# Optimization experiments

Measured on AMD Instinct MI355X. Metric: run time of the kernel, lower is better.

## Reference

```python
import jax, jax.numpy as jnp
import numpy as np

EMB_DIM = 1024
HEAD = 16
HEAD_DIM = EMB_DIM // HEAD


def setup_inputs() -> dict:
    key = jax.random.key(0)
    ks = jax.random.split(key, 6)
    s = 1.0 / np.sqrt(EMB_DIM)
    return {
        "z": jax.random.normal(ks[0], (4, 2048, EMB_DIM), dtype=jnp.float32),
        "w_q": jax.random.normal(ks[1], (EMB_DIM, EMB_DIM), dtype=jnp.float32) * s,
        "w_k": jax.random.normal(ks[2], (EMB_DIM, EMB_DIM), dtype=jnp.float32) * s,
        "w_v": jax.random.normal(ks[3], (EMB_DIM, EMB_DIM), dtype=jnp.float32) * s,
        "w_o": jax.random.normal(ks[4], (EMB_DIM, EMB_DIM), dtype=jnp.float32) * s,
        "b_o": jax.random.normal(ks[5], (EMB_DIM,), dtype=jnp.float32) * 0.01,
    }


def reference(z, w_q, w_k, w_v, w_o, b_o):
    B, N, D = z.shape
    # QKV projections (nn.Linear: x @ W.T; here weights stored as (D_in, D_out))
    q = (z @ w_q).reshape(B, N, HEAD, HEAD_DIM).transpose(0, 2, 1, 3)  # bhnd
    k = (z @ w_k).reshape(B, N, HEAD, HEAD_DIM).transpose(0, 2, 1, 3)
    v = (z @ w_v).reshape(B, N, HEAD, HEAD_DIM).transpose(0, 2, 1, 3)
    scale = 1.0 / np.sqrt(HEAD_DIM).astype(np.float32)
    dots = jnp.einsum("bhnd,bhmd->bhnm", q, k) * scale
    attn = jax.nn.softmax(dots, axis=-1)
    out = jnp.einsum("bhnm,bhmd->bhnd", attn, v)
    out = out.transpose(0, 2, 1, 3).reshape(B, N, D)
    return out @ w_o + b_o
```

## Files before the change

### kernel.cpp

```cpp
#include <hip/hip_runtime.h>
#include <hip/hip_bf16.h>
#include <stdint.h>

typedef unsigned short u16;
typedef __attribute__((ext_vector_type(8))) short bf16x8;
typedef __attribute__((ext_vector_type(4))) float f32x4;
typedef __attribute__((ext_vector_type(16))) float f32x16;

static __device__ inline u16 f2bf(float f) {
  union { float f; uint32_t u; } v; v.f = f;
  uint32_t u = v.u;
  u += 0x7fffu + ((u >> 16) & 1);
  return (u16)(u >> 16);
}

static __device__ inline float fast_exp2(float x) {
#if __has_builtin(__builtin_amdgcn_exp2f)
  return __builtin_amdgcn_exp2f(x);
#else
  return __expf(x * 0.6931471805599453f);
#endif
}

static __device__ inline uint32_t pack_bf16(float lo, float hi) {
#if __has_builtin(__builtin_amdgcn_cvt_pk_bf16_f32)
  typedef __attribute__((ext_vector_type(2))) __bf16 bf16x2_t;
  bf16x2_t r = __builtin_amdgcn_cvt_pk_bf16_f32(lo, hi);
  union { bf16x2_t v; uint32_t u; } c; c.v = r;
  return c.u;
#else
  union { float f; uint32_t u; } a, b;
  a.f = lo; b.f = hi;
  uint32_t ua = a.u + 0x8000u;
  uint32_t ub = b.u + 0x8000u;
  return __builtin_amdgcn_perm(ub, ua, 0x07060302u);
#endif
}

static __device__ __forceinline__ void plswap(uint32_t a, uint32_t b,
                                              uint32_t& x, uint32_t& y) {
#if __has_builtin(__builtin_amdgcn_permlane32_swap)
  auto r = __builtin_amdgcn_permlane32_swap(a, b, false, false);
  x = (uint32_t)r[0]; y = (uint32_t)r[1];
#else
  int h = (threadIdx.x & 63) >> 5;
  uint32_t pa = (uint32_t)__shfl_xor((int)a, 32, 64);
  uint32_t pb = (uint32_t)__shfl_xor((int)b, 32, 64);
  x = h ? pb : a;
  y = h ? b : pa;
#endif
}

static __device__ __forceinline__ void load_lds_128(const u16* g, u16* l) {
  __builtin_amdgcn_global_load_lds((const __attribute__((address_space(1))) void*)g,
                                   (__attribute__((address_space(3))) void*)l,
                                   16, 0, 0);
}

__global__ __launch_bounds__(256) void prep_kernel(const float* __restrict__ zsrc,
                                                   u16* __restrict__ zdst,
                                                   const float* __restrict__ wq,
                                                   const float* __restrict__ wk,
                                                   const float* __restrict__ wv,
                                                   const float* __restrict__ wo,
                                                   u16* __restrict__ bqkv,
                                                   u16* __restrict__ wot) {
  const int bid = blockIdx.x;
  const int tid = threadIdx.x;
  if (bid < 8192) {
    int i = bid * 256 + tid;
    float4 v = reinterpret_cast<const float4*>(zsrc)[i];
    uint2 o;
    o.x = pack_bf16(v.x, v.y);
    o.y = pack_bf16(v.z, v.w);
    reinterpret_cast<uint2*>(zdst)[i] = o;
    return;
  }
  const int w = bid - 8192;
  const int z = w >> 10;
  const int rem = w & 1023;
  const float* src = (z == 0) ? wq : (z == 1) ? wk : (z == 2) ? wv : wo;
  u16* dst = (z < 3) ? (bqkv + (size_t)z * 1024 * 1024) : wot;
  __shared__ float tile[32][33];
  const int c0 = (rem & 31) * 32, r0 = (rem >> 5) * 32;
  const int tx = tid & 31, ty = tid >> 5;
#pragma unroll
  for (int i = 0; i < 32; i += 8)
    tile[ty + i][tx] = src[(size_t)(r0 + ty + i) * 1024 + c0 + tx];
  __syncthreads();
#pragma unroll
  for (int i = 0; i < 32; i += 8)
    dst[(size_t)(c0 + ty + i) * 1024 + r0 + tx] = f2bf(tile[tx][ty + i]);
}

__global__ __launch_bounds__(256) void gemm_bt64_kernel(
    const u16* __restrict__ A, const u16* __restrict__ Bt,
    float* __restrict__ outC, const float* __restrict__ bias) {
  const int Kd = 1024;
  const int n0 = blockIdx.x * 64;
  const int m0 = blockIdx.y * 128;
  __shared__ __align__(16) u16 Asm[128 * 32];
  __shared__ __align__(16) u16 Bsm[64 * 32];
  const int tid = threadIdx.x;
  const int wave = tid >> 6, lane = tid & 63;
  const int quad = lane >> 4, l15 = lane & 15;
  const int wm = (wave >> 1) * 64, wn = (wave & 1) * 32;

  const int c0 = wave * 128 + lane;
  const int c1 = c0 + 64;
  const int r0 = c0 >> 2, p0 = (c0 & 3) * 8;
  const int r1 = c1 >> 2, p1 = (c1 & 3) * 8;
  const int cB = tid;
  const int rB = cB >> 2, pB = (cB & 3) * 8;

  const u16* Ab = A + (size_t)m0 * Kd;
  const u16* Bb = Bt + (size_t)n0 * Kd;

  f32x4 acc[4][2] = {};

  for (int k0 = 0; k0 < Kd; k0 += 32) {
    __syncthreads();
    load_lds_128(Ab + (size_t)r0 * Kd + k0 + p0, Asm + c0 * 8);
    load_lds_128(Ab + (size_t)r1 * Kd + k0 + p1, Asm + c1 * 8);
    load_lds_128(Bb + (size_t)rB * Kd + k0 + pB, Bsm + cB * 8);
    __syncthreads();
    bf16x8 af[4], bf[2];
#pragma unroll
    for (int i = 0; i < 4; i++)
      af[i] = *reinterpret_cast<const bf16x8*>(Asm + (wm + i * 16 + l15) * 32 + quad * 8);
#pragma unroll
    for (int i = 0; i < 2; i++)
      bf[i] = *reinterpret_cast<const bf16x8*>(Bsm + (wn + i * 16 + l15) * 32 + quad * 8);
#pragma unroll
    for (int mi = 0; mi < 4; mi++)
#pragma unroll
      for (int ni = 0; ni < 2; ni++)
        acc[mi][ni] = __builtin_amdgcn_mfma_f32_16x16x32_bf16(af[mi], bf[ni], acc[mi][ni], 0, 0, 0);
  }

#pragma unroll
  for (int mi = 0; mi < 4; mi++)
#pragma unroll
    for (int ni = 0; ni < 2; ni++) {
      int n = n0 + wn + ni * 16 + l15;
      float bv = bias[n];
#pragma unroll
      for (int r = 0; r < 4; r++) {
        int m = m0 + wm + mi * 16 + quad * 4 + r;
        outC[(size_t)m * 1024 + n] = acc[mi][ni][r] + bv;
      }
    }
}

__global__ __launch_bounds__(512, 2) void gemm256_kernel(
    const u16* __restrict__ A, const u16* __restrict__ Bt,
    u16* __restrict__ outQ, u16* __restrict__ outK, u16* __restrict__ outVt) {
  const int tid = threadIdx.x;
  const int lane = tid & 63;
  const int wave = tid >> 6;
  const int quad = lane >> 4, l15 = lane & 15;
  const int e15 = l15 & 7;
  const int wm = wave >> 2;
  const int wn = wave & 3;

  unsigned lin = blockIdx.y * gridDim.x + blockIdx.x;
  unsigned nwg = gridDim.x * gridDim.y;
  lin = (lin & 7u) * (nwg >> 3) + (lin >> 3);
  const int bx = lin % gridDim.x, by = lin / gridDim.x;
  const int n0 = bx * 256, m0 = by * 256;

  __shared__ __align__(16) u16 AsmL[2][16384];
  __shared__ __align__(16) u16 BsmL[2][16384];
  u16* const As_[2] = {&AsmL[0][0], &AsmL[1][0]};
  u16* const Bs_[2] = {&BsmL[0][0], &BsmL[1][0]};

  const u16* Abase = A + (size_t)m0 * 1024;
  const u16* Bbase = Bt + (size_t)n0 * 1024;

  const int awoff = wm * 8192;
  const int bwoff = (wn >> 1) * 8192 + (wn & 1) * 4096;

  f32x4 acc[8][4] = {};
  bf16x8 af[4][2], bfr[4][2];

#define STG_HALF(ldsp, gp)                                                      \
  {                                                                             \
    const int cs0 = tid, cs1 = tid + 512;                                       \
    const int r0_ = cs0 >> 3, g0_ = (((cs0 & 7) ^ (r0_ & 7)) << 3);             \
    const int r1_ = cs1 >> 3, g1_ = (((cs1 & 7) ^ (r1_ & 7)) << 3);             \
    load_lds_128((gp) + (size_t)r0_ * 1024 + g0_, (ldsp) + cs0 * 8);            \
    load_lds_128((gp) + (size_t)r1_ * 1024 + g1_, (ldsp) + cs1 * 8);            \
  }

#define PHB() do { asm volatile("" ::: "memory"); __builtin_amdgcn_s_barrier(); \
                   asm volatile("" ::: "memory"); } while (0)
#define LGKM0() do { asm volatile("s_waitcnt lgkmcnt(0)" ::: "memory");         \
                     __builtin_amdgcn_sched_barrier(0); } while (0)
#define VMC8()  asm volatile("s_waitcnt vmcnt(8)" ::: "memory")

#define RD_A(mb, B)                                                             \
  _Pragma("unroll") for (int x = 0; x < 4; x++)                                 \
  _Pragma("unroll") for (int kk = 0; kk < 2; kk++)                              \
    af[x][kk] = *reinterpret_cast<const bf16x8*>(                               \
        As_[B] + awoff + (((mb) + x) * 16 + l15) * 64 + (((quad + kk * 4) ^ e15) << 3));

#define RD_B(nb, B)                                                             \
  _Pragma("unroll") for (int x = 0; x < 2; x++)                                 \
  _Pragma("unroll") for (int kk = 0; kk < 2; kk++)                              \
    bfr[(nb) + x][kk] = *reinterpret_cast<const bf16x8*>(                       \
        Bs_[B] + bwoff + (((nb) + x) * 16 + l15) * 64 + (((quad + kk * 4) ^ e15) << 3));

#define MM(mb, nb)                                                              \
  _Pragma("unroll") for (int kk = 0; kk < 2; kk++)                              \
  _Pragma("unroll") for (int x = 0; x < 4; x++)                                 \
  _Pragma("unroll") for (int y = 0; y < 2; y++)                                 \
    acc[(mb) + x][(nb) + y] = __builtin_amdgcn_mfma_f32_16x16x32_bf16(          \
        af[x][kk], bfr[(nb) + y][kk], acc[(mb) + x][(nb) + y], 0, 0, 0);

#define TILE4(B, KS)                                                            \
  RD_A(0, B); RD_B(0, B);                                                       \
  PHB(); LGKM0(); __builtin_amdgcn_s_setprio(1); MM(0, 0);                      \
  __builtin_amdgcn_s_setprio(0); PHB();                                         \
  RD_B(2, B);                                                                   \
  PHB(); LGKM0(); __builtin_amdgcn_s_setprio(1); MM(0, 2);                      \
  __builtin_amdgcn_s_setprio(0); PHB();                                         \
  RD_A(4, B);                                                                   \
  STG_HALF(Bs_[B], Bbase + (KS)); STG_HALF(Bs_[B] + 8192, Bbase + 128 * 1024 + (KS)); \
  PHB(); LGKM0(); __builtin_amdgcn_s_setprio(1); MM(4, 0);                      \
  __builtin_amdgcn_s_setprio(0); PHB();                                         \
  STG_HALF(As_[B], Abase + (KS)); STG_HALF(As_[B] + 8192, Abase + 128 * 1024 + (KS)); \
  PHB(); __builtin_amdgcn_s_setprio(1); MM(4, 2);                               \
  __builtin_amdgcn_s_setprio(0); VMC8(); PHB();

  STG_HALF(As_[0], Abase);      STG_HALF(As_[0] + 8192, Abase + 128 * 1024);
  STG_HALF(Bs_[0], Bbase);      STG_HALF(Bs_[0] + 8192, Bbase + 128 * 1024);
  STG_HALF(As_[1], Abase + 64); STG_HALF(As_[1] + 8192, Abase + 128 * 1024 + 64);
  STG_HALF(Bs_[1], Bbase + 64); STG_HALF(Bs_[1] + 8192, Bbase + 128 * 1024 + 64);
  VMC8(); PHB();

#pragma unroll 1
  for (int it = 0; it < 8; ++it) {
    int t2 = it * 2 + 2; if (t2 > 15) t2 = 15;
    int t3 = it * 2 + 3; if (t3 > 15) t3 = 15;
    const int k2 = t2 * 64, k3 = t3 * 64;
    TILE4(0, k2);
    TILE4(1, k3);
  }

  const int which = (n0 + wn * 64) >> 10;
#pragma unroll
  for (int mi = 0; mi < 8; mi++)
#pragma unroll
    for (int ni = 0; ni < 4; ni++) {
      int n = n0 + wn * 64 + ni * 16 + l15;
      int hn = n & 1023;
      int hh = hn >> 6, dim = hn & 63;
      if (which == 2) {
        int m = m0 + wm * 128 + mi * 16 + quad * 4;
        int b = m >> 11, tok = m & 2047;
        uint2 pk;
        pk.x = pack_bf16(acc[mi][ni][0], acc[mi][ni][1]);
        pk.y = pack_bf16(acc[mi][ni][2], acc[mi][ni][3]);
        *reinterpret_cast<uint2*>(outVt + ((size_t)(b * 16 + hh) * 64 + dim) * 2048 + tok) = pk;
      } else {
        u16* dst = (which == 0) ? outQ : outK;
        float qscale = (which == 0) ? 0.1803368801111204f : 1.0f;
#pragma unroll
        for (int r = 0; r < 4; r++) {
          int m = m0 + wm * 128 + mi * 16 + quad * 4 + r;
          int b = m >> 11, tok = m & 2047;
          dst[(((size_t)(b * 16 + hh)) * 2048 + tok) * 64 + dim] = f2bf(acc[mi][ni][r] * qscale);
        }
      }
    }
#undef STG_HALF
#undef PHB
#undef LGKM0
#undef VMC8
#undef RD_A
#undef RD_B
#undef MM
#undef TILE4
}

__global__ __launch_bounds__(256, 2) void attn_kernel(const u16* __restrict__ Q,
                                                      const u16* __restrict__ K,
                                                      const u16* __restrict__ Vt,
                                                      u16* __restrict__ Oout) {
  const int bh = blockIdx.x;
  const int q0 = blockIdx.y * 256;
  const int tid = threadIdx.x;
  const int wave = tid >> 6, lane = tid & 63;
  const int l31 = lane & 31, h = lane >> 5;
  const int e = l31 & 7;

  __shared__ __align__(16) u16 Kb2[2][4096];
  __shared__ __align__(16) u16 Vb2[2][4096];

  const u16* Qg = Q + ((size_t)bh * 2048 + q0 + wave * 64) * 64;
  const u16* Kg = K + (size_t)bh * 2048 * 64;
  const u16* Vg = Vt + (size_t)bh * 64 * 2048;

  bf16x8 qf[2][4];
#pragma unroll
  for (int j = 0; j < 2; j++)
#pragma unroll
    for (int dc = 0; dc < 4; dc++)
      qf[j][dc] = *reinterpret_cast<const bf16x8*>(
          Qg + (size_t)(j * 32 + l31) * 64 + dc * 16 + h * 8);

  const int s0 = tid, s1 = tid + 256;
  const int sr0 = s0 >> 3, sg0 = ((s0 & 7) ^ (sr0 & 7)) * 8;
  const int sr1 = s1 >> 3, sg1 = ((s1 & 7) ^ (sr1 & 7)) * 8;

  load_lds_128(Kg + (size_t)sr0 * 64 + sg0, &Kb2[0][s0 * 8]);
  load_lds_128(Kg + (size_t)sr1 * 64 + sg1, &Kb2[0][s1 * 8]);
  load_lds_128(Vg + (size_t)sr0 * 2048 + sg0, &Vb2[0][s0 * 8]);
  load_lds_128(Vg + (size_t)sr1 * 2048 + sg1, &Vb2[0][s1 * 8]);
  __syncthreads();

  float ls[2][2] = {};
  f32x16 oacc[2][2] = {};
  int cur = 0;

  for (int kt = 0; kt < 2048; kt += 64) {
    const u16* uK = &Kb2[cur][0];
    const u16* uV = &Vb2[cur][0];

    bf16x8 kfr[2][4], vfr[2][2][2];
#pragma unroll
    for (int kb = 0; kb < 2; kb++)
#pragma unroll
      for (int dc = 0; dc < 4; dc++)
        kfr[kb][dc] = *reinterpret_cast<const bf16x8*>(
            uK + (kb * 32 + l31) * 64 + (((2 * dc + h) ^ e) * 8));
#pragma unroll
    for (int dt = 0; dt < 2; dt++)
#pragma unroll
      for (int kb = 0; kb < 2; kb++)
#pragma unroll
        for (int kc = 0; kc < 2; kc++)
          vfr[dt][kb][kc] = *reinterpret_cast<const bf16x8*>(
              uV + (dt * 32 + l31) * 64 + (((4 * kb + 2 * kc + h) ^ e) * 8));

    if (kt + 64 < 2048) {
      const int nb = cur ^ 1;
      load_lds_128(Kg + (size_t)(kt + 64 + sr0) * 64 + sg0, &Kb2[nb][s0 * 8]);
      load_lds_128(Kg + (size_t)(kt + 64 + sr1) * 64 + sg1, &Kb2[nb][s1 * 8]);
      load_lds_128(Vg + (size_t)sr0 * 2048 + kt + 64 + sg0, &Vb2[nb][s0 * 8]);
      load_lds_128(Vg + (size_t)sr1 * 2048 + kt + 64 + sg1, &Vb2[nb][s1 * 8]);
    }

    f32x16 s4[4];
    __builtin_amdgcn_s_setprio(1);
#pragma unroll
    for (int g = 0; g < 4; g++) {
      const int kb = g >> 1, j = g & 1;
      f32x16 s = {};
#pragma unroll
      for (int dc = 0; dc < 4; dc++)
        s = __builtin_amdgcn_mfma_f32_32x32x16_bf16(kfr[kb][dc], qf[j][dc], s, 0, 0, 0);
      s4[g] = s;
    }
    __builtin_amdgcn_s_setprio(0);

#pragma unroll
    for (int g = 0; g < 4; g++) {
      const int kb = g >> 1, j = g & 1;
      float p[16];
#pragma unroll
      for (int i = 0; i < 16; i++) p[i] = fast_exp2(s4[g][i]);
#pragma unroll
      for (int i = 0; i < 16; i += 2) { ls[j][0] += p[i]; ls[j][1] += p[i + 1]; }
      uint32_t pk[4][2];
#pragma unroll
      for (int rq = 0; rq < 4; rq++) {
        pk[rq][0] = pack_bf16(p[rq * 4 + 0], p[rq * 4 + 1]);
        pk[rq][1] = pack_bf16(p[rq * 4 + 2], p[rq * 4 + 3]);
      }
      uint4 b0, b1;
      plswap(pk[0][0], pk[1][0], b0.x, b0.z);
      plswap(pk[0][1], pk[1][1], b0.y, b0.w);
      plswap(pk[2][0], pk[3][0], b1.x, b1.z);
      plswap(pk[2][1], pk[3][1], b1.y, b1.w);
      union { uint4 u; bf16x8 v; } bf0, bf1;
      bf0.u = b0; bf1.u = b1;
      __builtin_amdgcn_s_setprio(1);
#pragma unroll
      for (int dt = 0; dt < 2; dt++) {
        oacc[j][dt] = __builtin_amdgcn_mfma_f32_32x32x16_bf16(vfr[dt][kb][0], bf0.v, oacc[j][dt], 0, 0, 0);
        oacc[j][dt] = __builtin_amdgcn_mfma_f32_32x32x16_bf16(vfr[dt][kb][1], bf1.v, oacc[j][dt], 0, 0, 0);
      }
      __builtin_amdgcn_s_setprio(0);
    }

    __syncthreads();
    cur ^= 1;
  }

  const int b = bh >> 4, hd = bh & 15;
  u16* dst = Oout + (size_t)b * 2048 * 1024 + (size_t)hd * 64;
#pragma unroll
  for (int j = 0; j < 2; j++) {
    float lsum = ls[j][0] + ls[j][1];
    lsum += __shfl_xor(lsum, 32, 64);
    float inv = __builtin_amdgcn_rcpf(lsum);
    const size_t qrow = (size_t)(q0 + wave * 64 + j * 32 + l31) * 1024;
#pragma unroll
    for (int dt = 0; dt < 2; dt++)
#pragma unroll
      for (int rq = 0; rq < 4; rq++) {
        uint2 o;
        o.x = pack_bf16(oacc[j][dt][rq * 4 + 0] * inv, oacc[j][dt][rq * 4 + 1] * inv);
        o.y = pack_bf16(oacc[j][dt][rq * 4 + 2] * inv, oacc[j][dt][rq * 4 + 3] * inv);
        *reinterpret_cast<uint2*>(dst + qrow + dt * 32 + rq * 8 + h * 4) = o;
      }
  }
}

extern "C" void kernel_launch(void* const* d_in, const int* in_sizes, int n_in,
                              void* d_out, int out_size, void* d_ws, size_t ws_size,
                              hipStream_t stream) {
  (void)in_sizes; (void)n_in; (void)out_size; (void)ws_size;
  const float* z  = (const float*)d_in[0];
  const float* wq = (const float*)d_in[1];
  const float* wk = (const float*)d_in[2];
  const float* wv = (const float*)d_in[3];
  const float* wo = (const float*)d_in[4];
  const float* bo = (const float*)d_in[5];
  float* out = (float*)d_out;

  char* ws = (char*)d_ws;
  u16* zb   = (u16*)(ws);
  u16* bqkv = (u16*)(ws + (16ull << 20));
  u16* wot  = (u16*)(ws + (22ull << 20));
  u16* Qb   = (u16*)(ws + (24ull << 20));
  u16* Kb   = (u16*)(ws + (40ull << 20));
  u16* Vtb  = (u16*)(ws + (56ull << 20));
  u16* Ob   = zb;

  prep_kernel<<<12288, 256, 0, stream>>>(z, zb, wq, wk, wv, wo, bqkv, wot);
  gemm256_kernel<<<dim3(12, 32), 512, 0, stream>>>(zb, bqkv, Qb, Kb, Vtb);
  attn_kernel<<<dim3(64, 8), 256, 0, stream>>>(Qb, Kb, Vtb, Ob);
  gemm_bt64_kernel<<<dim3(16, 64), 256, 0, stream>>>(Ob, wot, out, bo);
}
```

Baseline: 280.9 us.

## Split QKV GEMM into Q/K and V launches with transposed MFMA for packed stores

The fused QKV projection GEMM becomes a template launched twice: once for the Q/K columns and once for the V columns. In the Q/K variant the MFMA operands are swapped, so each lane holds four consecutive head dimensions of one token and can write them as a single packed 8-byte store instead of four scattered 2-byte stores. The output GEMM also gets the same XCD-aware block index swizzle already used by the QKV GEMM. The cost is an extra kernel launch and a smaller V-only grid (128 blocks) that may underfill the GPU.

```diff
diff --git a/kernel.cpp b/kernel.cpp
--- a/kernel.cpp
+++ b/kernel.cpp
@@ -97,8 +97,11 @@
     const u16* __restrict__ A, const u16* __restrict__ Bt,
     float* __restrict__ outC, const float* __restrict__ bias) {
   const int Kd = 1024;
-  const int n0 = blockIdx.x * 64;
-  const int m0 = blockIdx.y * 128;
+  unsigned lin = blockIdx.y * gridDim.x + blockIdx.x;
+  unsigned nwg = gridDim.x * gridDim.y;
+  lin = (lin & 7u) * (nwg >> 3) + (lin >> 3);
+  const int n0 = (lin % gridDim.x) * 64;
+  const int m0 = (lin / gridDim.x) * 128;
   __shared__ __align__(16) u16 Asm[128 * 32];
   __shared__ __align__(16) u16 Bsm[64 * 32];
   const int tid = threadIdx.x;
@@ -152,6 +155,7 @@
     }
 }
 
+template <int VT>
 __global__ __launch_bounds__(512, 2) void gemm256_kernel(
     const u16* __restrict__ A, const u16* __restrict__ Bt,
     u16* __restrict__ outQ, u16* __restrict__ outK, u16* __restrict__ outVt) {
@@ -167,7 +171,8 @@
   unsigned nwg = gridDim.x * gridDim.y;
   lin = (lin & 7u) * (nwg >> 3) + (lin >> 3);
   const int bx = lin % gridDim.x, by = lin / gridDim.x;
-  const int n0 = bx * 256, m0 = by * 256;
+  const int n0 = (VT ? 2048 : 0) + bx * 256;
+  const int m0 = by * 256;
 
   __shared__ __align__(16) u16 AsmL[2][16384];
   __shared__ __align__(16) u16 BsmL[2][16384];
@@ -213,9 +218,14 @@
 #define MM(mb, nb)                                                              \
   _Pragma("unroll") for (int kk = 0; kk < 2; kk++)                              \
   _Pragma("unroll") for (int x = 0; x < 4; x++)                                 \
-  _Pragma("unroll") for (int y = 0; y < 2; y++)                                 \
-    acc[(mb) + x][(nb) + y] = __builtin_amdgcn_mfma_f32_16x16x32_bf16(          \
-        af[x][kk], bfr[(nb) + y][kk], acc[(mb) + x][(nb) + y], 0, 0, 0);
+  _Pragma("unroll") for (int y = 0; y < 2; y++) {                               \
+    if (VT)                                                                     \
+      acc[(mb) + x][(nb) + y] = __builtin_amdgcn_mfma_f32_16x16x32_bf16(        \
+          af[x][kk], bfr[(nb) + y][kk], acc[(mb) + x][(nb) + y], 0, 0, 0);      \
+    else                                                                        \
+      acc[(mb) + x][(nb) + y] = __builtin_amdgcn_mfma_f32_16x16x32_bf16(        \
+          bfr[(nb) + y][kk], af[x][kk], acc[(mb) + x][(nb) + y], 0, 0, 0);      \
+  }
 
 #define TILE4(B, KS)                                                            \
   RD_A(0, B); RD_B(0, B);                                                       \
@@ -247,32 +257,41 @@
     TILE4(1, k3);
   }
 
-  const int which = (n0 + wn * 64) >> 10;
-#pragma unroll
-  for (int mi = 0; mi < 8; mi++)
-#pragma unroll
-    for (int ni = 0; ni < 4; ni++) {
-      int n = n0 + wn * 64 + ni * 16 + l15;
-      int hn = n & 1023;
-      int hh = hn >> 6, dim = hn & 63;
-      if (which == 2) {
+  if (VT) {
+#pragma unroll
+    for (int mi = 0; mi < 8; mi++)
+#pragma unroll
+      for (int ni = 0; ni < 4; ni++) {
+        int n = n0 + wn * 64 + ni * 16 + l15;
+        int hn = n & 1023;
+        int hh = hn >> 6, dim = hn & 63;
         int m = m0 + wm * 128 + mi * 16 + quad * 4;
         int b = m >> 11, tok = m & 2047;
         uint2 pk;
         pk.x = pack_bf16(acc[mi][ni][0], acc[mi][ni][1]);
         pk.y = pack_bf16(acc[mi][ni][2], acc[mi][ni][3]);
         *reinterpret_cast<uint2*>(outVt + ((size_t)(b * 16 + hh) * 64 + dim) * 2048 + tok) = pk;
-      } else {
-        u16* dst = (which == 0) ? outQ : outK;
-        float qscale = (which == 0) ? 0.1803368801111204f : 1.0f;
-#pragma unroll
-        for (int r = 0; r < 4; r++) {
-          int m = m0 + wm * 128 + mi * 16 + quad * 4 + r;
-          int b = m >> 11, tok = m & 2047;
-          dst[(((size_t)(b * 16 + hh)) * 2048 + tok) * 64 + dim] = f2bf(acc[mi][ni][r] * qscale);
-        }
+      }
+  } else {
+    const int which = (n0 + wn * 64) >> 10;
+    u16* dst0 = which ? outK : outQ;
+    const float qscale = which ? 1.0f : 0.1803368801111204f;
+    const int hh = ((n0 + wn * 64) & 1023) >> 6;
+#pragma unroll
+    for (int mi = 0; mi < 8; mi++) {
+      int mrow = m0 + wm * 128 + mi * 16 + l15;
+      int b = mrow >> 11, tok = mrow & 2047;
+      u16* drow = dst0 + ((size_t)(b * 16 + hh) * 2048 + tok) * 64;
+#pragma unroll
+      for (int ni = 0; ni < 4; ni++) {
+        int dim0 = ni * 16 + quad * 4;
+        uint2 o;
+        o.x = pack_bf16(acc[mi][ni][0] * qscale, acc[mi][ni][1] * qscale);
+        o.y = pack_bf16(acc[mi][ni][2] * qscale, acc[mi][ni][3] * qscale);
+        *reinterpret_cast<uint2*>(drow + dim0) = o;
       }
     }
+  }
 #undef STG_HALF
 #undef PHB
 #undef LGKM0
@@ -440,7 +459,8 @@
   u16* Ob   = zb;
 
   prep_kernel<<<12288, 256, 0, stream>>>(z, zb, wq, wk, wv, wo, bqkv, wot);
-  gemm256_kernel<<<dim3(12, 32), 512, 0, stream>>>(zb, bqkv, Qb, Kb, Vtb);
+  gemm256_kernel<0><<<dim3(8, 32), 512, 0, stream>>>(zb, bqkv, Qb, Kb, Vtb);
+  gemm256_kernel<1><<<dim3(4, 32), 512, 0, stream>>>(zb, bqkv, Qb, Kb, Vtb);
   attn_kernel<<<dim3(64, 8), 256, 0, stream>>>(Qb, Kb, Vtb, Ob);
   gemm_bt64_kernel<<<dim3(16, 64), 256, 0, stream>>>(Ob, wot, out, bo);
 }
```

New measurement: 287.4 us. 2.3% more time.

## Triple-buffer K/V tiles in attention with prefetch two tiles ahead

Applied to the files above, without the earlier changes.

Moves the attention kernel's K/V shared-memory staging from double to triple buffering, issuing async loads two iterations ahead. It waits with a partial vmcnt and uses one barrier per iteration at the loop top instead of a full __syncthreads at the end. The aim is to hide global-load latency behind more compute. In exchange, LDS use rises to 48KB per block, which may limit occupancy. The last iterations issue dummy reloads of tile 0 so the wait count stays uniform.

```diff
diff --git a/kernel.cpp b/kernel.cpp
--- a/kernel.cpp
+++ b/kernel.cpp
@@ -294,8 +294,8 @@
   const int l31 = lane & 31, h = lane >> 5;
   const int e = l31 & 7;
 
-  __shared__ __align__(16) u16 Kb2[2][4096];
-  __shared__ __align__(16) u16 Vb2[2][4096];
+  __shared__ __align__(16) u16 Kb3[3][4096];
+  __shared__ __align__(16) u16 Vb3[3][4096];
 
   const u16* Qg = Q + ((size_t)bh * 2048 + q0 + wave * 64) * 64;
   const u16* Kg = K + (size_t)bh * 2048 * 64;
@@ -313,19 +313,34 @@
   const int sr0 = s0 >> 3, sg0 = ((s0 & 7) ^ (sr0 & 7)) * 8;
   const int sr1 = s1 >> 3, sg1 = ((s1 & 7) ^ (sr1 & 7)) * 8;
 
-  load_lds_128(Kg + (size_t)sr0 * 64 + sg0, &Kb2[0][s0 * 8]);
-  load_lds_128(Kg + (size_t)sr1 * 64 + sg1, &Kb2[0][s1 * 8]);
-  load_lds_128(Vg + (size_t)sr0 * 2048 + sg0, &Vb2[0][s0 * 8]);
-  load_lds_128(Vg + (size_t)sr1 * 2048 + sg1, &Vb2[0][s1 * 8]);
-  __syncthreads();
+#define STAGE(ktv, buf_)                                                           \
+  load_lds_128(Kg + (size_t)((ktv) + sr0) * 64 + sg0, &Kb3[buf_][s0 * 8]);         \
+  load_lds_128(Kg + (size_t)((ktv) + sr1) * 64 + sg1, &Kb3[buf_][s1 * 8]);         \
+  load_lds_128(Vg + (size_t)sr0 * 2048 + (ktv) + sg0, &Vb3[buf_][s0 * 8]);         \
+  load_lds_128(Vg + (size_t)sr1 * 2048 + (ktv) + sg1, &Vb3[buf_][s1 * 8]);
+
+  STAGE(0, 0);
+  STAGE(64, 1);
 
   float ls[2][2] = {};
   f32x16 oacc[2][2] = {};
-  int cur = 0;
+  int rbuf = 0;
 
   for (int kt = 0; kt < 2048; kt += 64) {
-    const u16* uK = &Kb2[cur][0];
-    const u16* uV = &Vb2[cur][0];
+    asm volatile("s_waitcnt vmcnt(4)" ::: "memory");
+    __builtin_amdgcn_sched_barrier(0);
+    asm volatile("" ::: "memory");
+    __builtin_amdgcn_s_barrier();
+    asm volatile("" ::: "memory");
+
+    const u16* uK = &Kb3[rbuf][0];
+    const u16* uV = &Vb3[rbuf][0];
+
+    {
+      int pbuf = rbuf + 2; if (pbuf >= 3) pbuf -= 3;
+      int ktp = kt + 128; if (ktp >= 2048) ktp = 0;
+      STAGE(ktp, pbuf);
+    }
 
     bf16x8 kfr[2][4], vfr[2][2][2];
 #pragma unroll
@@ -342,14 +357,6 @@
         for (int kc = 0; kc < 2; kc++)
           vfr[dt][kb][kc] = *reinterpret_cast<const bf16x8*>(
               uV + (dt * 32 + l31) * 64 + (((4 * kb + 2 * kc + h) ^ e) * 8));
-
-    if (kt + 64 < 2048) {
-      const int nb = cur ^ 1;
-      load_lds_128(Kg + (size_t)(kt + 64 + sr0) * 64 + sg0, &Kb2[nb][s0 * 8]);
-      load_lds_128(Kg + (size_t)(kt + 64 + sr1) * 64 + sg1, &Kb2[nb][s1 * 8]);
-      load_lds_128(Vg + (size_t)sr0 * 2048 + kt + 64 + sg0, &Vb2[nb][s0 * 8]);
-      load_lds_128(Vg + (size_t)sr1 * 2048 + kt + 64 + sg1, &Vb2[nb][s1 * 8]);
-    }
 
     f32x16 s4[4];
     __builtin_amdgcn_s_setprio(1);
@@ -394,9 +401,9 @@
       __builtin_amdgcn_s_setprio(0);
     }
 
-    __syncthreads();
-    cur ^= 1;
-  }
+    rbuf = (rbuf == 2) ? 0 : rbuf + 1;
+  }
+#undef STAGE
 
   const int b = bh >> 4, hd = bh & 15;
   u16* dst = Oout + (size_t)b * 2048 * 1024 + (size_t)hd * 64;
```

Result: slower. 288.3 us (+2.6%).

## Shrink QKV GEMM tile to 256x128 and simplify the double-buffer pipeline

Applied to the files above, without the earlier changes.

Changes the QKV projection GEMM from 256x256 tiles to 256x128 tiles, doubling the grid to 768 workgroups and using a 4x2 wave layout with half the accumulators per wave. The staging schedule is rewritten so each K-step issues all global-to-LDS loads for the next buffer up front, then waits with vmcnt(6) before computing the current buffer in two MFMA phases. The goal is better CU occupancy and load balance on a GPU with many CUs, plus lower register and LDS pressure. The cost is lower arithmetic intensity per tile, since each A tile is now reloaded twice as often.

```diff
diff --git a/kernel.cpp b/kernel.cpp
--- a/kernel.cpp
+++ b/kernel.cpp
@@ -152,7 +152,7 @@
     }
 }
 
-__global__ __launch_bounds__(512, 2) void gemm256_kernel(
+__global__ __launch_bounds__(512, 2) void gemm_qkv_kernel(
     const u16* __restrict__ A, const u16* __restrict__ Bt,
     u16* __restrict__ outQ, u16* __restrict__ outK, u16* __restrict__ outVt) {
   const int tid = threadIdx.x;
@@ -160,103 +160,114 @@
   const int wave = tid >> 6;
   const int quad = lane >> 4, l15 = lane & 15;
   const int e15 = l15 & 7;
-  const int wm = wave >> 2;
-  const int wn = wave & 3;
+  const int wm = wave >> 1;
+  const int wn = wave & 1;
 
   unsigned lin = blockIdx.y * gridDim.x + blockIdx.x;
   unsigned nwg = gridDim.x * gridDim.y;
   lin = (lin & 7u) * (nwg >> 3) + (lin >> 3);
   const int bx = lin % gridDim.x, by = lin / gridDim.x;
-  const int n0 = bx * 256, m0 = by * 256;
+  const int n0 = bx * 128, m0 = by * 256;
 
   __shared__ __align__(16) u16 AsmL[2][16384];
-  __shared__ __align__(16) u16 BsmL[2][16384];
+  __shared__ __align__(16) u16 BsmL[2][8192];
   u16* const As_[2] = {&AsmL[0][0], &AsmL[1][0]};
   u16* const Bs_[2] = {&BsmL[0][0], &BsmL[1][0]};
 
   const u16* Abase = A + (size_t)m0 * 1024;
   const u16* Bbase = Bt + (size_t)n0 * 1024;
 
-  const int awoff = wm * 8192;
-  const int bwoff = (wn >> 1) * 8192 + (wn & 1) * 4096;
-
-  f32x4 acc[8][4] = {};
+  const int awoff = wm * 4096;
+  const int bwoff = wn * 4096;
+
+  f32x4 acc[4][4] = {};
   bf16x8 af[4][2], bfr[4][2];
 
-#define STG_HALF(ldsp, gp)                                                      \
+#define STG_ALL(B_, KS)                                                         \
   {                                                                             \
-    const int cs0 = tid, cs1 = tid + 512;                                       \
-    const int r0_ = cs0 >> 3, g0_ = (((cs0 & 7) ^ (r0_ & 7)) << 3);             \
-    const int r1_ = cs1 >> 3, g1_ = (((cs1 & 7) ^ (r1_ & 7)) << 3);             \
-    load_lds_128((gp) + (size_t)r0_ * 1024 + g0_, (ldsp) + cs0 * 8);            \
-    load_lds_128((gp) + (size_t)r1_ * 1024 + g1_, (ldsp) + cs1 * 8);            \
+    _Pragma("unroll") for (int i_ = 0; i_ < 4; i_++) {                          \
+      const int c_ = tid + i_ * 512;                                            \
+      const int r_ = c_ >> 3, g_ = (((c_ & 7) ^ (r_ & 7)) << 3);                \
+      load_lds_128(Abase + (size_t)r_ * 1024 + (KS) + g_, As_[B_] + c_ * 8);    \
+    }                                                                           \
+    _Pragma("unroll") for (int i_ = 0; i_ < 2; i_++) {                          \
+      const int c_ = tid + i_ * 512;                                            \
+      const int r_ = c_ >> 3, g_ = (((c_ & 7) ^ (r_ & 7)) << 3);                \
+      load_lds_128(Bbase + (size_t)r_ * 1024 + (KS) + g_, Bs_[B_] + c_ * 8);    \
+    }                                                                           \
   }
 
 #define PHB() do { asm volatile("" ::: "memory"); __builtin_amdgcn_s_barrier(); \
                    asm volatile("" ::: "memory"); } while (0)
 #define LGKM0() do { asm volatile("s_waitcnt lgkmcnt(0)" ::: "memory");         \
                      __builtin_amdgcn_sched_barrier(0); } while (0)
-#define VMC8()  asm volatile("s_waitcnt vmcnt(8)" ::: "memory")
-
-#define RD_A(mb, B)                                                             \
-  _Pragma("unroll") for (int x = 0; x < 4; x++)                                 \
+#define VMC6() do { asm volatile("s_waitcnt vmcnt(6)" ::: "memory");            \
+                    __builtin_amdgcn_sched_barrier(0); } while (0)
+
+#define RD_A01(B)                                                               \
+  _Pragma("unroll") for (int x = 0; x < 2; x++)                                 \
   _Pragma("unroll") for (int kk = 0; kk < 2; kk++)                              \
     af[x][kk] = *reinterpret_cast<const bf16x8*>(                               \
-        As_[B] + awoff + (((mb) + x) * 16 + l15) * 64 + (((quad + kk * 4) ^ e15) << 3));
-
-#define RD_B(nb, B)                                                             \
+        As_[B] + awoff + (x * 16 + l15) * 64 + (((quad + kk * 4) ^ e15) << 3));
+
+#define RD_A23(B)                                                               \
+  _Pragma("unroll") for (int x = 2; x < 4; x++)                                 \
+  _Pragma("unroll") for (int kk = 0; kk < 2; kk++)                              \
+    af[x][kk] = *reinterpret_cast<const bf16x8*>(                               \
+        As_[B] + awoff + (x * 16 + l15) * 64 + (((quad + kk * 4) ^ e15) << 3));
+
+#define RD_B(B)                                                                 \
+  _Pragma("unroll") for (int y = 0; y < 4; y++)                                 \
+  _Pragma("unroll") for (int kk = 0; kk < 2; kk++)                              \
+    bfr[y][kk] = *reinterpret_cast<const bf16x8*>(                              \
+        Bs_[B] + bwoff + (y * 16 + l15) * 64 + (((quad + kk * 4) ^ e15) << 3));
+
+#define MM01()                                                                  \
+  _Pragma("unroll") for (int kk = 0; kk < 2; kk++)                              \
   _Pragma("unroll") for (int x = 0; x < 2; x++)                                 \
+  _Pragma("unroll") for (int y = 0; y < 4; y++)                                 \
+    acc[x][y] = __builtin_amdgcn_mfma_f32_16x16x32_bf16(                        \
+        af[x][kk], bfr[y][kk], acc[x][y], 0, 0, 0);
+
+#define MM23()                                                                  \
   _Pragma("unroll") for (int kk = 0; kk < 2; kk++)                              \
-    bfr[(nb) + x][kk] = *reinterpret_cast<const bf16x8*>(                       \
-        Bs_[B] + bwoff + (((nb) + x) * 16 + l15) * 64 + (((quad + kk * 4) ^ e15) << 3));
-
-#define MM(mb, nb)                                                              \
-  _Pragma("unroll") for (int kk = 0; kk < 2; kk++)                              \
-  _Pragma("unroll") for (int x = 0; x < 4; x++)                                 \
-  _Pragma("unroll") for (int y = 0; y < 2; y++)                                 \
-    acc[(mb) + x][(nb) + y] = __builtin_amdgcn_mfma_f32_16x16x32_bf16(          \
-        af[x][kk], bfr[(nb) + y][kk], acc[(mb) + x][(nb) + y], 0, 0, 0);
-
-#define TILE4(B, KS)                                                            \
-  RD_A(0, B); RD_B(0, B);                                                       \
-  PHB(); LGKM0(); __builtin_amdgcn_s_setprio(1); MM(0, 0);                      \
+  _Pragma("unroll") for (int x = 2; x < 4; x++)                                 \
+  _Pragma("unroll") for (int y = 0; y < 4; y++)                                 \
+    acc[x][y] = __builtin_amdgcn_mfma_f32_16x16x32_bf16(                        \
+        af[x][kk], bfr[y][kk], acc[x][y], 0, 0, 0);
+
+#define TILE2(B, KSNEXT)                                                        \
+  STG_ALL(B ^ 1, KSNEXT);                                                       \
+  VMC6(); PHB();                                                                \
+  RD_A01(B); RD_B(B);                                                           \
+  PHB(); LGKM0(); __builtin_amdgcn_s_setprio(1); MM01();                        \
   __builtin_amdgcn_s_setprio(0); PHB();                                         \
-  RD_B(2, B);                                                                   \
-  PHB(); LGKM0(); __builtin_amdgcn_s_setprio(1); MM(0, 2);                      \
-  __builtin_amdgcn_s_setprio(0); PHB();                                         \
-  RD_A(4, B);                                                                   \
-  STG_HALF(Bs_[B], Bbase + (KS)); STG_HALF(Bs_[B] + 8192, Bbase + 128 * 1024 + (KS)); \
-  PHB(); LGKM0(); __builtin_amdgcn_s_setprio(1); MM(4, 0);                      \
-  __builtin_amdgcn_s_setprio(0); PHB();                                         \
-  STG_HALF(As_[B], Abase + (KS)); STG_HALF(As_[B] + 8192, Abase + 128 * 1024 + (KS)); \
-  PHB(); __builtin_amdgcn_s_setprio(1); MM(4, 2);                               \
-  __builtin_amdgcn_s_setprio(0); VMC8(); PHB();
-
-  STG_HALF(As_[0], Abase);      STG_HALF(As_[0] + 8192, Abase + 128 * 1024);
-  STG_HALF(Bs_[0], Bbase);      STG_HALF(Bs_[0] + 8192, Bbase + 128 * 1024);
-  STG_HALF(As_[1], Abase + 64); STG_HALF(As_[1] + 8192, Abase + 128 * 1024 + 64);
-  STG_HALF(Bs_[1], Bbase + 64); STG_HALF(Bs_[1] + 8192, Bbase + 128 * 1024 + 64);
-  VMC8(); PHB();
+  RD_A23(B);                                                                    \
+  PHB(); LGKM0(); __builtin_amdgcn_s_setprio(1); MM23();                        \
+  __builtin_amdgcn_s_setprio(0); PHB();
+
+  STG_ALL(0, 0);
 
 #pragma unroll 1
   for (int it = 0; it < 8; ++it) {
-    int t2 = it * 2 + 2; if (t2 > 15) t2 = 15;
-    int t3 = it * 2 + 3; if (t3 > 15) t3 = 15;
-    const int k2 = t2 * 64, k3 = t3 * 64;
-    TILE4(0, k2);
-    TILE4(1, k3);
+    const int t0 = it * 2;
+    int tn1 = t0 + 1;
+    int tn2 = t0 + 2; if (tn2 > 15) tn2 = 15;
+    const int k1 = tn1 * 64, k2 = tn2 * 64;
+    TILE2(0, k1);
+    TILE2(1, k2);
   }
 
   const int which = (n0 + wn * 64) >> 10;
 #pragma unroll
-  for (int mi = 0; mi < 8; mi++)
+  for (int mi = 0; mi < 4; mi++)
 #pragma unroll
     for (int ni = 0; ni < 4; ni++) {
       int n = n0 + wn * 64 + ni * 16 + l15;
       int hn = n & 1023;
       int hh = hn >> 6, dim = hn & 63;
       if (which == 2) {
-        int m = m0 + wm * 128 + mi * 16 + quad * 4;
+        int m = m0 + wm * 64 + mi * 16 + quad * 4;
         int b = m >> 11, tok = m & 2047;
         uint2 pk;
         pk.x = pack_bf16(acc[mi][ni][0], acc[mi][ni][1]);
@@ -267,20 +278,22 @@
         float qscale = (which == 0) ? 0.1803368801111204f : 1.0f;
 #pragma unroll
         for (int r = 0; r < 4; r++) {
-          int m = m0 + wm * 128 + mi * 16 + quad * 4 + r;
+          int m = m0 + wm * 64 + mi * 16 + quad * 4 + r;
           int b = m >> 11, tok = m & 2047;
           dst[(((size_t)(b * 16 + hh)) * 2048 + tok) * 64 + dim] = f2bf(acc[mi][ni][r] * qscale);
         }
       }
     }
-#undef STG_HALF
+#undef STG_ALL
 #undef PHB
 #undef LGKM0
-#undef VMC8
-#undef RD_A
+#undef VMC6
+#undef RD_A01
+#undef RD_A23
 #undef RD_B
-#undef MM
-#undef TILE4
+#undef MM01
+#undef MM23
+#undef TILE2
 }
 
 __global__ __launch_bounds__(256, 2) void attn_kernel(const u16* __restrict__ Q,
@@ -440,7 +453,7 @@
   u16* Ob   = zb;
 
   prep_kernel<<<12288, 256, 0, stream>>>(z, zb, wq, wk, wv, wo, bqkv, wot);
-  gemm256_kernel<<<dim3(12, 32), 512, 0, stream>>>(zb, bqkv, Qb, Kb, Vtb);
+  gemm_qkv_kernel<<<dim3(24, 32), 512, 0, stream>>>(zb, bqkv, Qb, Kb, Vtb);
   attn_kernel<<<dim3(64, 8), 256, 0, stream>>>(Qb, Kb, Vtb, Ob);
   gemm_bt64_kernel<<<dim3(16, 64), 256, 0, stream>>>(Ob, wot, out, bo);
 }
```

Result: slower. 289.2 us (+2.9%).
